# Kernel optimization log

Hardware: AMD Instinct MI355X
Metric: run time of the kernel (lower is better)

The kernel has to match this reference:

```python
import jax, jax.numpy as jnp
import numpy as np

N = 100_000      # nodes
E = 1_600_000    # nonzeros of the rescaled Laplacian (avg degree 16)
F_IN = 128
F_OUT = 128
K = 4


def setup_inputs() -> dict:
    key = jax.random.key(0)
    ks = jax.random.split(key, 6)
    x = jax.random.normal(ks[0], (N, F_IN), dtype=jnp.float32)
    filter_coeff = jax.random.normal(ks[1], (K, N), dtype=jnp.float32)
    # glorot-ish scale for [K, F_in, F_out]
    stdv = float(np.sqrt(6.0 / (F_IN + F_OUT)))
    weight = jax.random.uniform(ks[2], (K, F_IN, F_OUT), dtype=jnp.float32,
                                minval=-stdv, maxval=stdv)
    bias = jnp.zeros((F_OUT,), dtype=jnp.float32)
    src = jax.random.randint(ks[3], (E,), 0, N, dtype=jnp.int32)
    dst = jax.random.randint(ks[4], (E,), 0, N, dtype=jnp.int32)
    # edge values of L_hat = 2L/lambda_max - I (precomputed sparse matrix)
    edge_w = jax.random.normal(ks[5], (E,), dtype=jnp.float32) * 0.1
    return {"x": x, "filter_coeff": filter_coeff, "weight": weight,
            "bias": bias, "edge_w": edge_w, "src": src, "dst": dst}


def reference(x, filter_coeff, weight, bias, edge_w, src, dst):
    n = x.shape[0]

    def spmm(h):  # edge-weighted gather-scale-segment_sum == dgl.update_all
        return jax.ops.segment_sum(h[src] * edge_w[:, None], dst,
                                   num_segments=n)

    # Chebyshev recurrence: T0 = x, T1 = L_hat x, T_k = 2 L_hat T_{k-1} - T_{k-2}
    Tx0 = x
    out = (filter_coeff[0][:, None] * Tx0) @ weight[0]
    Tx1 = spmm(x)
    out = out + (filter_coeff[1][:, None] * Tx1) @ weight[1]
    for k in range(2, weight.shape[0]):
        Tx2 = 2.0 * spmm(Tx1) - Tx0
        out = out + (filter_coeff[k][:, None] * Tx2) @ weight[k]
        Tx0, Tx1 = Tx1, Tx2
    return out + bias
```

## Files before the change

### kernel.cpp

```cpp
#include <hip/hip_runtime.h>
#include <hip/hip_bf16.h>
#include <cstdio>

#define F 128
#define BSHIFT 9
#define BROWS 512
#define C2 4096

typedef __attribute__((ext_vector_type(4))) float f32x4;
typedef __attribute__((ext_vector_type(4))) unsigned short u16x4;
typedef __attribute__((ext_vector_type(8))) short s16x8;

__device__ inline unsigned short f2bf(float x) {
  unsigned int u = __float_as_uint(x);
  u += 0x7fffu + ((u >> 16) & 1u);
  return (unsigned short)(u >> 16);
}
__device__ inline float bf2f(unsigned int h) {
  return __uint_as_float(h << 16);
}

__global__ void bucket_hist_kernel(const int* __restrict__ dst, int* __restrict__ bhist,
                                   int E, int B) {
  __shared__ int h[256];
  int t = threadIdx.x;
  h[t] = 0;
  __syncthreads();
  for (int e = blockIdx.x * blockDim.x + t; e < E; e += gridDim.x * blockDim.x)
    atomicAdd(&h[dst[e] >> BSHIFT], 1);
  __syncthreads();
  if (t < B && h[t]) atomicAdd(&bhist[t], h[t]);
}

__global__ void bucket_scan_kernel(const int* __restrict__ bhist, int* __restrict__ bbase,
                                   int* __restrict__ bcursor, int* __restrict__ rp,
                                   int E, int B, int N) {
  __shared__ int sm[256];
  int t = threadIdx.x;
  int v = (t < B) ? bhist[t] : 0;
  sm[t] = v;
  __syncthreads();
  int x = v;
  for (int off = 1; off < 256; off <<= 1) {
    int add = (t >= off) ? sm[t - off] : 0;
    __syncthreads();
    x += add;
    sm[t] = x;
    __syncthreads();
  }
  int excl = x - v;
  if (t < B) { bbase[t] = excl; bcursor[t] = excl; }
  if (t == 0) { bbase[B] = E; rp[N] = E; }
}

__global__ __launch_bounds__(256) void bucket_scatter_kernel(
    const int* __restrict__ src, const int* __restrict__ dst, const float* __restrict__ ew,
    int* __restrict__ bcursor, unsigned int* __restrict__ stg_p, float* __restrict__ stg_w,
    int E, int B) {
  __shared__ int hist[256], gbase[256], cur[256], sm[256], scn[256];
  __shared__ unsigned int sp[C2];
  __shared__ float swt[C2];
  __shared__ int sdest[C2];
  int t = threadIdx.x;
  int e0 = blockIdx.x * C2;
  int cnt = min(C2, E - e0);
  hist[t] = 0;
  __syncthreads();
#pragma unroll
  for (int i = 0; i < C2 / 256; ++i) {
    int e = e0 + t + i * 256;
    if (e < E) atomicAdd(&hist[dst[e] >> BSHIFT], 1);
  }
  __syncthreads();
  int v = hist[t];
  gbase[t] = (t < B && v) ? atomicAdd(&bcursor[t], v) : 0;
  sm[t] = v;
  __syncthreads();
  int x = v;
  for (int off = 1; off < 256; off <<= 1) {
    int add = (t >= off) ? sm[t - off] : 0;
    __syncthreads();
    x += add;
    sm[t] = x;
    __syncthreads();
  }
  scn[t] = x - v;
  cur[t] = 0;
  __syncthreads();
#pragma unroll
  for (int i = 0; i < C2 / 256; ++i) {
    int e = e0 + t + i * 256;
    if (e < E) {
      int d = dst[e];
      int b = d >> BSHIFT;
      int r = atomicAdd(&cur[b], 1);
      int slot = scn[b] + r;
      sp[slot] = (unsigned int)src[e] | ((unsigned int)(d & (BROWS - 1)) << 17);
      swt[slot] = ew[e];
      sdest[slot] = gbase[b] + r;
    }
  }
  __syncthreads();
#pragma unroll
  for (int i = 0; i < C2 / 256; ++i) {
    int s = t + i * 256;
    if (s < cnt) {
      int dpos = sdest[s];
      stg_p[dpos] = sp[s];
      stg_w[dpos] = swt[s];
    }
  }
}

__global__ __launch_bounds__(256) void csr_build_kernel(
    const unsigned int* __restrict__ stg_p, const float* __restrict__ stg_w,
    const int* __restrict__ bbase, int* __restrict__ rp, int2* __restrict__ csr,
    int N, int B) {
  __shared__ int rhist[BROWS], rloc[BROWS], curp[BROWS];
  __shared__ int sm[256];
  int b = blockIdx.x, t = threadIdx.x;
  int row0 = b << BSHIFT;
  int base = bbase[b];
  int cnt = bbase[b + 1] - base;
  rhist[t] = 0;
  rhist[t + 256] = 0;
  __syncthreads();
  for (int s = base + t; s < base + cnt; s += 256)
    atomicAdd(&rhist[stg_p[s] >> 17], 1);
  __syncthreads();
  int a0 = rhist[2 * t], a1 = rhist[2 * t + 1];
  int pv = a0 + a1;
  sm[t] = pv;
  __syncthreads();
  int x = pv;
  for (int off = 1; off < 256; off <<= 1) {
    int add = (t >= off) ? sm[t - off] : 0;
    __syncthreads();
    x += add;
    sm[t] = x;
    __syncthreads();
  }
  int pexcl = x - pv;
  int r0 = 2 * t, r1 = 2 * t + 1;
  rloc[r0] = pexcl;
  rloc[r1] = pexcl + a0;
  if (row0 + r0 < N) rp[row0 + r0] = base + rloc[r0];
  if (row0 + r1 < N) rp[row0 + r1] = base + rloc[r1];
  curp[r0] = base + rloc[r0];
  curp[r1] = base + rloc[r1];
  __syncthreads();
  for (int s = base + t; s < base + cnt; s += 256) {
    unsigned int p = stg_p[s];
    int dl = p >> 17;
    int pos = atomicAdd(&curp[dl], 1);
    int2 entry;
    entry.x = (int)(p & 0x1ffffu);
    entry.y = __float_as_int(stg_w[s]);
    csr[pos] = entry;
  }
}

__global__ void convx_kernel(const float* __restrict__ x, unsigned short* __restrict__ xbf,
                             int total4) {
  int i = blockIdx.x * 256 + threadIdx.x;
  if (i >= total4) return;
  f32x4 v = ((const f32x4*)x)[i];
  u16x4 o;
  o.x = f2bf(v.x); o.y = f2bf(v.y); o.z = f2bf(v.z); o.w = f2bf(v.w);
  ((u16x4*)xbf)[i] = o;
}

__global__ __launch_bounds__(256) void spmm_kernel(
    const unsigned short* __restrict__ Tin, const unsigned short* __restrict__ Tsub,
    unsigned short* __restrict__ Tout, const int* __restrict__ rp,
    const int2* __restrict__ csr, int n, float scale) {
  int wv = blockIdx.x * (blockDim.x >> 6) + (threadIdx.x >> 6);
  if (wv >= n) return;
  int lane = threadIdx.x & 63;
  int sl = lane & 15;
  int eo = lane >> 4;
  int j0 = rp[wv], end = rp[wv + 1];
  const uint4* Tin4 = (const uint4*)Tin;
  float acc[8];
#pragma unroll
  for (int c = 0; c < 8; ++c) acc[c] = 0.f;

  for (int j = j0; j < end; j += 16) {
    int2 e[4];
    float w[4];
    uint4 v[4];
#pragma unroll
    for (int u = 0; u < 4; ++u) {
      int je = j + 4 * u + eo;
      bool live = je < end;
      e[u] = csr[live ? je : end - 1];
      w[u] = live ? __int_as_float(e[u].y) : 0.f;
    }
#pragma unroll
    for (int u = 0; u < 4; ++u) v[u] = Tin4[(size_t)e[u].x * 16 + sl];
#pragma unroll
    for (int u = 0; u < 4; ++u) {
      acc[0] = fmaf(w[u], bf2f(v[u].x & 0xffffu), acc[0]);
      acc[1] = fmaf(w[u], bf2f(v[u].x >> 16), acc[1]);
      acc[2] = fmaf(w[u], bf2f(v[u].y & 0xffffu), acc[2]);
      acc[3] = fmaf(w[u], bf2f(v[u].y >> 16), acc[3]);
      acc[4] = fmaf(w[u], bf2f(v[u].z & 0xffffu), acc[4]);
      acc[5] = fmaf(w[u], bf2f(v[u].z >> 16), acc[5]);
      acc[6] = fmaf(w[u], bf2f(v[u].w & 0xffffu), acc[6]);
      acc[7] = fmaf(w[u], bf2f(v[u].w >> 16), acc[7]);
    }
  }
#pragma unroll
  for (int h = 16; h <= 32; h <<= 1)
#pragma unroll
    for (int c = 0; c < 8; ++c) acc[c] += __shfl_xor(acc[c], h, 64);

  if (eo == 0) {
    float r[8];
#pragma unroll
    for (int c = 0; c < 8; ++c) r[c] = scale * acc[c];
    if (Tsub) {
      uint4 p = ((const uint4*)Tsub)[(size_t)wv * 16 + sl];
      r[0] -= bf2f(p.x & 0xffffu); r[1] -= bf2f(p.x >> 16);
      r[2] -= bf2f(p.y & 0xffffu); r[3] -= bf2f(p.y >> 16);
      r[4] -= bf2f(p.z & 0xffffu); r[5] -= bf2f(p.z >> 16);
      r[6] -= bf2f(p.w & 0xffffu); r[7] -= bf2f(p.w >> 16);
    }
    uint4 o;
    o.x = (unsigned)f2bf(r[0]) | ((unsigned)f2bf(r[1]) << 16);
    o.y = (unsigned)f2bf(r[2]) | ((unsigned)f2bf(r[3]) << 16);
    o.z = (unsigned)f2bf(r[4]) | ((unsigned)f2bf(r[5]) << 16);
    o.w = (unsigned)f2bf(r[6]) | ((unsigned)f2bf(r[7]) << 16);
    ((uint4*)Tout)[(size_t)wv * 16 + sl] = o;
  }
}

__global__ void convw_kernel(const float* __restrict__ W, unsigned short* __restrict__ Wf,
                             int total) {
  int idx = blockIdx.x * 256 + threadIdx.x;
  if (idx >= total) return;
  int j = idx & 7;
  int lane = (idx >> 3) & 63;
  int nt = (idx >> 9) & 7;
  int kk = (idx >> 12) & 3;
  int ks = idx >> 14;
  int kl = kk * 32 + (lane >> 4) * 8 + j;
  int col = nt * 16 + (lane & 15);
  Wf[idx] = f2bf(W[(size_t)ks * F * F + (size_t)kl * F + col]);
}

struct GemmArgs {
  const unsigned short* A[8];
  const float* fc;
  const unsigned short* Wt;
  const float* bias;
  float* out;
  int n;
  int kslices;
};

__global__ __launch_bounds__(256, 4) void gemm_kernel(GemmArgs args) {
  const int t = threadIdx.x;
  const int lane = t & 63;
  const int wid = t >> 6;
  const int wrow = wid >> 1, wcol = wid & 1;
  const int n = args.n;
  const int r0 = blockIdx.x * 64 + wrow * 32;
  if (r0 >= n) return;
  const int arow = lane & 15;
  const int kg = lane >> 4;

  f32x4 Cf[2][4];
#pragma unroll
  for (int mt = 0; mt < 2; ++mt)
#pragma unroll
    for (int nt = 0; nt < 4; ++nt) Cf[mt][nt] = (f32x4){0.f, 0.f, 0.f, 0.f};

  int row_a[2];
#pragma unroll
  for (int mt = 0; mt < 2; ++mt) {
    int r = r0 + mt * 16 + arow;
    row_a[mt] = r < n ? r : n - 1;
  }

  for (int ks = 0; ks < args.kslices; ++ks) {
    const unsigned short* As = args.A[ks];
    const unsigned short* Wfb = args.Wt + (size_t)ks * 16384 + (wcol * 4) * 512 + lane * 8;
    f32x4 acc[2][4];
#pragma unroll
    for (int mt = 0; mt < 2; ++mt)
#pragma unroll
      for (int nt = 0; nt < 4; ++nt) acc[mt][nt] = (f32x4){0.f, 0.f, 0.f, 0.f};

#pragma unroll
    for (int kk = 0; kk < 4; ++kk) {
      s16x8 af[2], bfr[4];
#pragma unroll
      for (int mt = 0; mt < 2; ++mt)
        af[mt] = *(const s16x8*)(As + (size_t)row_a[mt] * F + kk * 32 + kg * 8);
#pragma unroll
      for (int nt = 0; nt < 4; ++nt)
        bfr[nt] = *(const s16x8*)(Wfb + (kk * 8 + nt) * 512);
#pragma unroll
      for (int mt = 0; mt < 2; ++mt)
#pragma unroll
        for (int nt = 0; nt < 4; ++nt)
          acc[mt][nt] = __builtin_amdgcn_mfma_f32_16x16x32_bf16(af[mt], bfr[nt],
                                                                acc[mt][nt], 0, 0, 0);
    }

#pragma unroll
    for (int mt = 0; mt < 2; ++mt) {
      int row = r0 + mt * 16 + kg * 4;
      f32x4 fv;
      if (row + 3 < n) {
        fv = *(const f32x4*)(args.fc + (size_t)ks * n + row);
      } else {
#pragma unroll
        for (int r4 = 0; r4 < 4; ++r4) {
          int rr = row + r4;
          if (rr >= n) rr = n - 1;
          fv[r4] = args.fc[(size_t)ks * n + rr];
        }
      }
#pragma unroll
      for (int nt = 0; nt < 4; ++nt) Cf[mt][nt] += fv * acc[mt][nt];
    }
  }

#pragma unroll
  for (int nt = 0; nt < 4; ++nt) {
    int col = (wcol * 4 + nt) * 16 + arow;
    float bv = args.bias[col];
#pragma unroll
    for (int mt = 0; mt < 2; ++mt) {
#pragma unroll
      for (int r4 = 0; r4 < 4; ++r4) {
        int row = r0 + mt * 16 + kg * 4 + r4;
        if (row < n) args.out[(size_t)row * F + col] = Cf[mt][nt][r4] + bv;
      }
    }
  }
}

extern "C" void kernel_launch(void* const* d_in, const int* in_sizes, int n_in,
                              void* d_out, int out_size, void* d_ws, size_t ws_size,
                              hipStream_t stream) {
  const float* x    = (const float*)d_in[0];
  const float* fc   = (const float*)d_in[1];
  const float* W    = (const float*)d_in[2];
  const float* bias = (const float*)d_in[3];
  const float* ew   = (const float*)d_in[4];
  const int*   src  = (const int*)d_in[5];
  const int*   dst  = (const int*)d_in[6];

  const int N = in_sizes[0] / F;
  const int K = in_sizes[2] / (F * F);
  const int E = in_sizes[4];
  const int B = (N + BROWS - 1) >> BSHIFT;

  size_t off = 0;
  char* base = (char*)d_ws;
  auto alloc = [&](size_t bytes) -> void* {
    void* p = base + off;
    off += (bytes + 511) & ~(size_t)511;
    return p;
  };
  int* rp              = (int*)alloc(((size_t)N + 1) * 4);
  int* bhist           = (int*)alloc(1024);
  int* bbase           = (int*)alloc(1040);
  int* bcursor         = (int*)alloc(1024);
  int2* csr            = (int2*)alloc((size_t)E * 8);
  unsigned short* Wt   = (unsigned short*)alloc((size_t)K * F * F * 2);
  unsigned short* xbf  = (unsigned short*)alloc((size_t)N * F * 2);
  unsigned short* T[8];
  T[0] = xbf;
  for (int k = 1; k < K && k < 8; ++k) T[k] = (unsigned short*)alloc((size_t)N * F * 2);
  unsigned int* stg_p;
  float* stg_w;
  if (K >= 3 && (size_t)N * F * 2 >= (size_t)E * 8) {
    stg_p = (unsigned int*)T[2];
    stg_w = (float*)(T[2] + (size_t)E * 2);
  } else {
    stg_p = (unsigned int*)alloc((size_t)E * 4);
    stg_w = (float*)alloc((size_t)E * 4);
  }
  if (off > ws_size) {
    fprintf(stderr, "kernel_launch: ws too small: need %zu have %zu\n", off, ws_size);
    return;
  }

  hipMemsetAsync(bhist, 0, 1024, stream);
  int hblocks = (E + 255) / 256;
  if (hblocks > 2048) hblocks = 2048;
  hipLaunchKernelGGL(bucket_hist_kernel, dim3(hblocks), dim3(256), 0, stream, dst, bhist, E, B);
  hipLaunchKernelGGL(bucket_scan_kernel, dim3(1), dim3(256), 0, stream, bhist, bbase, bcursor,
                     rp, E, B, N);
  int sblocks = (E + C2 - 1) / C2;
  hipLaunchKernelGGL(bucket_scatter_kernel, dim3(sblocks), dim3(256), 0, stream, src, dst, ew,
                     bcursor, stg_p, stg_w, E, B);
  hipLaunchKernelGGL(csr_build_kernel, dim3(B), dim3(256), 0, stream, stg_p, stg_w, bbase,
                     rp, csr, N, B);

  int total4 = N * F / 4;
  hipLaunchKernelGGL(convx_kernel, dim3((total4 + 255) / 256), dim3(256), 0, stream,
                     x, xbf, total4);

  int sb = (N + 3) / 4;
  if (K > 1)
    hipLaunchKernelGGL(spmm_kernel, dim3(sb), dim3(256), 0, stream, xbf,
                       (const unsigned short*)nullptr, T[1], rp, csr, N, 1.0f);
  for (int k = 2; k < K; ++k) {
    const unsigned short* prev = T[k - 2];
    hipLaunchKernelGGL(spmm_kernel, dim3(sb), dim3(256), 0, stream, T[k - 1], prev, T[k],
                       rp, csr, N, 2.0f);
  }

  int total = K * F * F;
  hipLaunchKernelGGL(convw_kernel, dim3((total + 255) / 256), dim3(256), 0, stream, W, Wt,
                     total);

  GemmArgs ga;
  for (int k = 0; k < 8; ++k) ga.A[k] = (k < K) ? T[k] : xbf;
  ga.fc = fc; ga.Wt = Wt; ga.bias = bias;
  ga.out = (float*)d_out;
  ga.n = N; ga.kslices = K;
  hipLaunchKernelGGL(gemm_kernel, dim3((N + 63) / 64), dim3(256), 0, stream, ga);
}
```

Baseline: 361.8 us.

## Map SpMM rows to 16-lane groups and stage GEMM weights in LDS

The SpMM kernel now gives each row to 16 lanes instead of a full 64-lane wavefront. This removes the cross-lane shuffle reduction and the padded edge slots, and puts four rows in each wave. The GEMM kernel copies each weight slice into shared memory with asynchronous global-to-LDS loads, so the waves in a block share one copy instead of each reading it from global memory. This adds two block barriers per slice and 32 KB of LDS per block, which may limit occupancy. The SpMM change also exposes less memory parallelism per row, since each lane group processes four edges at a time serially.

```diff
diff --git a/kernel.cpp b/kernel.cpp
--- a/kernel.cpp
+++ b/kernel.cpp
@@ -18,6 +18,12 @@
 }
 __device__ inline float bf2f(unsigned int h) {
   return __uint_as_float(h << 16);
+}
+
+__device__ inline void async_load16(const void* g, void* l) {
+  __builtin_amdgcn_global_load_lds(
+      (const __attribute__((address_space(1))) void*)g,
+      (__attribute__((address_space(3))) void*)l, 16, 0, 0);
 }
 
 __global__ void bucket_hist_kernel(const int* __restrict__ dst, int* __restrict__ bhist,
@@ -174,65 +180,53 @@
     const unsigned short* __restrict__ Tin, const unsigned short* __restrict__ Tsub,
     unsigned short* __restrict__ Tout, const int* __restrict__ rp,
     const int2* __restrict__ csr, int n, float scale) {
-  int wv = blockIdx.x * (blockDim.x >> 6) + (threadIdx.x >> 6);
-  if (wv >= n) return;
-  int lane = threadIdx.x & 63;
-  int sl = lane & 15;
-  int eo = lane >> 4;
-  int j0 = rp[wv], end = rp[wv + 1];
+  int row = blockIdx.x * 16 + (threadIdx.x >> 4);
+  if (row >= n) return;
+  int sl = threadIdx.x & 15;
+  int j0 = rp[row], end = rp[row + 1];
   const uint4* Tin4 = (const uint4*)Tin;
   float acc[8];
 #pragma unroll
   for (int c = 0; c < 8; ++c) acc[c] = 0.f;
 
-  for (int j = j0; j < end; j += 16) {
+  for (int j = j0; j < end; j += 4) {
     int2 e[4];
-    float w[4];
-    uint4 v[4];
+#pragma unroll
+    for (int u = 0; u < 4; ++u)
+      if (j + u < end) e[u] = csr[j + u];
 #pragma unroll
     for (int u = 0; u < 4; ++u) {
-      int je = j + 4 * u + eo;
-      bool live = je < end;
-      e[u] = csr[live ? je : end - 1];
-      w[u] = live ? __int_as_float(e[u].y) : 0.f;
-    }
-#pragma unroll
-    for (int u = 0; u < 4; ++u) v[u] = Tin4[(size_t)e[u].x * 16 + sl];
-#pragma unroll
-    for (int u = 0; u < 4; ++u) {
-      acc[0] = fmaf(w[u], bf2f(v[u].x & 0xffffu), acc[0]);
-      acc[1] = fmaf(w[u], bf2f(v[u].x >> 16), acc[1]);
-      acc[2] = fmaf(w[u], bf2f(v[u].y & 0xffffu), acc[2]);
-      acc[3] = fmaf(w[u], bf2f(v[u].y >> 16), acc[3]);
-      acc[4] = fmaf(w[u], bf2f(v[u].z & 0xffffu), acc[4]);
-      acc[5] = fmaf(w[u], bf2f(v[u].z >> 16), acc[5]);
-      acc[6] = fmaf(w[u], bf2f(v[u].w & 0xffffu), acc[6]);
-      acc[7] = fmaf(w[u], bf2f(v[u].w >> 16), acc[7]);
-    }
-  }
-#pragma unroll
-  for (int h = 16; h <= 32; h <<= 1)
-#pragma unroll
-    for (int c = 0; c < 8; ++c) acc[c] += __shfl_xor(acc[c], h, 64);
-
-  if (eo == 0) {
-    float r[8];
-#pragma unroll
-    for (int c = 0; c < 8; ++c) r[c] = scale * acc[c];
-    if (Tsub) {
-      uint4 p = ((const uint4*)Tsub)[(size_t)wv * 16 + sl];
-      r[0] -= bf2f(p.x & 0xffffu); r[1] -= bf2f(p.x >> 16);
-      r[2] -= bf2f(p.y & 0xffffu); r[3] -= bf2f(p.y >> 16);
-      r[4] -= bf2f(p.z & 0xffffu); r[5] -= bf2f(p.z >> 16);
-      r[6] -= bf2f(p.w & 0xffffu); r[7] -= bf2f(p.w >> 16);
-    }
-    uint4 o;
-    o.x = (unsigned)f2bf(r[0]) | ((unsigned)f2bf(r[1]) << 16);
-    o.y = (unsigned)f2bf(r[2]) | ((unsigned)f2bf(r[3]) << 16);
-    o.z = (unsigned)f2bf(r[4]) | ((unsigned)f2bf(r[5]) << 16);
-    o.w = (unsigned)f2bf(r[6]) | ((unsigned)f2bf(r[7]) << 16);
-    ((uint4*)Tout)[(size_t)wv * 16 + sl] = o;
-  }
+      if (j + u < end) {
+        uint4 v = Tin4[(size_t)e[u].x * 16 + sl];
+        float w = __int_as_float(e[u].y);
+        acc[0] = fmaf(w, bf2f(v.x & 0xffffu), acc[0]);
+        acc[1] = fmaf(w, bf2f(v.x >> 16), acc[1]);
+        acc[2] = fmaf(w, bf2f(v.y & 0xffffu), acc[2]);
+        acc[3] = fmaf(w, bf2f(v.y >> 16), acc[3]);
+        acc[4] = fmaf(w, bf2f(v.z & 0xffffu), acc[4]);
+        acc[5] = fmaf(w, bf2f(v.z >> 16), acc[5]);
+        acc[6] = fmaf(w, bf2f(v.w & 0xffffu), acc[6]);
+        acc[7] = fmaf(w, bf2f(v.w >> 16), acc[7]);
+      }
+    }
+  }
+
+  float r[8];
+#pragma unroll
+  for (int c = 0; c < 8; ++c) r[c] = scale * acc[c];
+  if (Tsub) {
+    uint4 p = ((const uint4*)Tsub)[(size_t)row * 16 + sl];
+    r[0] -= bf2f(p.x & 0xffffu); r[1] -= bf2f(p.x >> 16);
+    r[2] -= bf2f(p.y & 0xffffu); r[3] -= bf2f(p.y >> 16);
+    r[4] -= bf2f(p.z & 0xffffu); r[5] -= bf2f(p.z >> 16);
+    r[6] -= bf2f(p.w & 0xffffu); r[7] -= bf2f(p.w >> 16);
+  }
+  uint4 o;
+  o.x = (unsigned)f2bf(r[0]) | ((unsigned)f2bf(r[1]) << 16);
+  o.y = (unsigned)f2bf(r[2]) | ((unsigned)f2bf(r[3]) << 16);
+  o.z = (unsigned)f2bf(r[4]) | ((unsigned)f2bf(r[5]) << 16);
+  o.w = (unsigned)f2bf(r[6]) | ((unsigned)f2bf(r[7]) << 16);
+  ((uint4*)Tout)[(size_t)row * 16 + sl] = o;
 }
 
 __global__ void convw_kernel(const float* __restrict__ W, unsigned short* __restrict__ Wf,
@@ -260,15 +254,16 @@
 };
 
 __global__ __launch_bounds__(256, 4) void gemm_kernel(GemmArgs args) {
+  __shared__ __align__(16) unsigned short SB[16384];
   const int t = threadIdx.x;
   const int lane = t & 63;
   const int wid = t >> 6;
   const int wrow = wid >> 1, wcol = wid & 1;
   const int n = args.n;
   const int r0 = blockIdx.x * 64 + wrow * 32;
-  if (r0 >= n) return;
   const int arow = lane & 15;
   const int kg = lane >> 4;
+  const bool live = r0 < n;
 
   f32x4 Cf[2][4];
 #pragma unroll
@@ -280,54 +275,67 @@
 #pragma unroll
   for (int mt = 0; mt < 2; ++mt) {
     int r = r0 + mt * 16 + arow;
-    row_a[mt] = r < n ? r : n - 1;
+    row_a[mt] = (live && r < n) ? r : 0;
+    if (live && r >= n) row_a[mt] = n - 1;
   }
 
   for (int ks = 0; ks < args.kslices; ++ks) {
-    const unsigned short* As = args.A[ks];
-    const unsigned short* Wfb = args.Wt + (size_t)ks * 16384 + (wcol * 4) * 512 + lane * 8;
-    f32x4 acc[2][4];
-#pragma unroll
-    for (int mt = 0; mt < 2; ++mt)
-#pragma unroll
-      for (int nt = 0; nt < 4; ++nt) acc[mt][nt] = (f32x4){0.f, 0.f, 0.f, 0.f};
-
-#pragma unroll
-    for (int kk = 0; kk < 4; ++kk) {
-      s16x8 af[2], bfr[4];
+#pragma unroll
+    for (int i = 0; i < 8; ++i) {
+      int chunk = wid * 8 + i;
+      const void* g = (const void*)(args.Wt + (size_t)ks * 16384 + chunk * 512 + lane * 8);
+      void* l = (void*)(SB + chunk * 512);
+      async_load16(g, l);
+    }
+    __syncthreads();
+
+    if (live) {
+      const unsigned short* As = args.A[ks];
+      f32x4 acc[2][4];
 #pragma unroll
       for (int mt = 0; mt < 2; ++mt)
-        af[mt] = *(const s16x8*)(As + (size_t)row_a[mt] * F + kk * 32 + kg * 8);
-#pragma unroll
-      for (int nt = 0; nt < 4; ++nt)
-        bfr[nt] = *(const s16x8*)(Wfb + (kk * 8 + nt) * 512);
-#pragma unroll
-      for (int mt = 0; mt < 2; ++mt)
+#pragma unroll
+        for (int nt = 0; nt < 4; ++nt) acc[mt][nt] = (f32x4){0.f, 0.f, 0.f, 0.f};
+
+#pragma unroll
+      for (int kk = 0; kk < 4; ++kk) {
+        s16x8 af[2], bfr[4];
+#pragma unroll
+        for (int mt = 0; mt < 2; ++mt)
+          af[mt] = *(const s16x8*)(As + (size_t)row_a[mt] * F + kk * 32 + kg * 8);
 #pragma unroll
         for (int nt = 0; nt < 4; ++nt)
-          acc[mt][nt] = __builtin_amdgcn_mfma_f32_16x16x32_bf16(af[mt], bfr[nt],
-                                                                acc[mt][nt], 0, 0, 0);
-    }
-
-#pragma unroll
-    for (int mt = 0; mt < 2; ++mt) {
-      int row = r0 + mt * 16 + kg * 4;
-      f32x4 fv;
-      if (row + 3 < n) {
-        fv = *(const f32x4*)(args.fc + (size_t)ks * n + row);
-      } else {
-#pragma unroll
-        for (int r4 = 0; r4 < 4; ++r4) {
-          int rr = row + r4;
-          if (rr >= n) rr = n - 1;
-          fv[r4] = args.fc[(size_t)ks * n + rr];
+          bfr[nt] = *(const s16x8*)&SB[(kk * 8 + wcol * 4 + nt) * 512 + lane * 8];
+#pragma unroll
+        for (int mt = 0; mt < 2; ++mt)
+#pragma unroll
+          for (int nt = 0; nt < 4; ++nt)
+            acc[mt][nt] = __builtin_amdgcn_mfma_f32_16x16x32_bf16(af[mt], bfr[nt],
+                                                                  acc[mt][nt], 0, 0, 0);
+      }
+
+#pragma unroll
+      for (int mt = 0; mt < 2; ++mt) {
+        int row = r0 + mt * 16 + kg * 4;
+        f32x4 fv;
+        if (row + 3 < n) {
+          fv = *(const f32x4*)(args.fc + (size_t)ks * n + row);
+        } else {
+#pragma unroll
+          for (int r4 = 0; r4 < 4; ++r4) {
+            int rr = row + r4;
+            if (rr >= n) rr = n - 1;
+            fv[r4] = args.fc[(size_t)ks * n + rr];
+          }
         }
+#pragma unroll
+        for (int nt = 0; nt < 4; ++nt) Cf[mt][nt] += fv * acc[mt][nt];
       }
-#pragma unroll
-      for (int nt = 0; nt < 4; ++nt) Cf[mt][nt] += fv * acc[mt][nt];
-    }
-  }
-
+    }
+    __syncthreads();
+  }
+
+  if (!live) return;
 #pragma unroll
   for (int nt = 0; nt < 4; ++nt) {
     int col = (wcol * 4 + nt) * 16 + arow;
@@ -406,7 +414,7 @@
   hipLaunchKernelGGL(convx_kernel, dim3((total4 + 255) / 256), dim3(256), 0, stream,
                      x, xbf, total4);
 
-  int sb = (N + 3) / 4;
+  int sb = (N + 15) / 16;
   if (K > 1)
     hipLaunchKernelGGL(spmm_kernel, dim3(sb), dim3(256), 0, stream, xbf,
                        (const unsigned short*)nullptr, T[1], rp, csr, N, 1.0f);
```

New measurement: 381.8 us. +5.5%, slower.
